# Kernel tuning notes

Measured on AMD Instinct MI355X. Metric: run time of the kernel, lower is better.

## Reference

```python
import jax, jax.numpy as jnp
import numpy as np

B, D, C, L, H = 4096, 768, 512, 32, 256
E = C * L  # total flattened extension embeddings

def _l2norm(x, eps=1e-12):
    n = jnp.sqrt(jnp.sum(x * x, axis=-1, keepdims=True))
    return x / jnp.maximum(n, eps)

def setup_inputs() -> dict:
    key = jax.random.key(0)
    ks = jax.random.split(key, 8)
    text_feat = jax.random.normal(ks[0], (B, D), dtype=jnp.float32)
    img_feat = jax.random.normal(ks[1], (B, D), dtype=jnp.float32)
    ext_embs = _l2norm(jax.random.normal(ks[2], (E, D), dtype=jnp.float32))
    concept_names = _l2norm(jax.random.normal(ks[3], (C, D), dtype=jnp.float32))
    # each concept has exactly L extension embeddings; sorted segment ids
    segment_ids = jnp.repeat(jnp.arange(C, dtype=jnp.int32), L)
    W1 = jax.random.normal(ks[4], (C + D, H), dtype=jnp.float32) * (1.0 / np.sqrt(C + D))
    b1 = jnp.zeros((H,), dtype=jnp.float32)
    W2 = jax.random.normal(ks[5], (H, C), dtype=jnp.float32) * (1.0 / np.sqrt(H))
    b2 = jnp.zeros((C,), dtype=jnp.float32)
    alpha = jnp.float32(0.5)
    temperature = jnp.float32(0.07)
    return {"text_feat": text_feat, "img_feat": img_feat, "ext_embs": ext_embs,
            "segment_ids": segment_ids, "concept_names": concept_names,
            "W1": W1, "b1": b1, "W2": W2, "b2": b2,
            "alpha": alpha, "temperature": temperature}

def reference(text_feat, img_feat, ext_embs, segment_ids, concept_names,
              W1, b1, W2, b2, alpha, temperature):
    # query = normalize(text + img)
    q = _l2norm(text_feat + img_feat)                      # [B, D]
    # ragged per-concept max similarity: one big GEMM + segmented max
    sim = jnp.einsum('bd,ed->be', q, ext_embs)            # [B, E]
    prior = jax.ops.segment_max(sim.T, segment_ids,
                                num_segments=C,
                                indices_are_sorted=True).T  # [B, C]
    # small MLP -> temperature softmax -> weighted concept sum
    h = jax.nn.relu(jnp.concatenate([prior, q], axis=-1) @ W1 + b1)  # [B, H]
    logits = h @ W2 + b2                                   # [B, C]
    weights = jax.nn.softmax(logits / temperature, axis=-1)
    dyn_prompt = weights @ concept_names                   # [B, D]
    combined = text_feat + alpha * dyn_prompt
    return _l2norm(combined)
```

## Files before the change

kernel.cpp:

```cpp
#include <hip/hip_runtime.h>
#include <hip/hip_bf16.h>

typedef unsigned short bfu;
typedef __attribute__((ext_vector_type(4))) float f32x4;
typedef __attribute__((ext_vector_type(8))) short bf16x8;
typedef __attribute__((ext_vector_type(4))) int i32x4;
typedef __attribute__((ext_vector_type(8))) int i32x8;

__device__ __forceinline__ unsigned short f2bf(float f) {
    unsigned int u = __float_as_uint(f);
    u += 0x7FFFu + ((u >> 16) & 1u);
    return (unsigned short)(u >> 16);
}

__device__ __forceinline__ unsigned pack_fp8x4(float a, float b, float c, float d) {
    int u = __builtin_amdgcn_cvt_pk_fp8_f32(a, b, 0, false);
    u = __builtin_amdgcn_cvt_pk_fp8_f32(c, d, u, true);
    return (unsigned)u;
}

__device__ __forceinline__ void gload_lds16(const void* g, void* l) {
    __builtin_amdgcn_global_load_lds(
        (const __attribute__((address_space(1))) unsigned int*)g,
        (__attribute__((address_space(3))) unsigned int*)l, 16, 0, 0);
}

__device__ __forceinline__ float block_sum256(float v, float* sm) {
    #pragma unroll
    for (int off = 32; off; off >>= 1) v += __shfl_xor(v, off);
    int w = threadIdx.x >> 6;
    if ((threadIdx.x & 63) == 0) sm[w] = v;
    __syncthreads();
    float r = sm[0] + sm[1] + sm[2] + sm[3];
    __syncthreads();
    return r;
}

__device__ __forceinline__ float block_max256(float v, float* sm) {
    #pragma unroll
    for (int off = 32; off; off >>= 1) v = fmaxf(v, __shfl_xor(v, off));
    int w = threadIdx.x >> 6;
    if ((threadIdx.x & 63) == 0) sm[w] = v;
    __syncthreads();
    float r = fmaxf(fmaxf(sm[0], sm[1]), fmaxf(sm[2], sm[3]));
    __syncthreads();
    return r;
}

__global__ __launch_bounds__(256) void prep_kernel(const float* __restrict__ text,
                                                   const float* __restrict__ img,
                                                   bfu* __restrict__ X,
                                                   unsigned* __restrict__ Q8,
                                                   const float* __restrict__ ext,
                                                   unsigned* __restrict__ E8,
                                                   const float* __restrict__ W1, bfu* __restrict__ W1t,
                                                   const float* __restrict__ W2, bfu* __restrict__ W2t,
                                                   const float* __restrict__ cn, bfu* __restrict__ cnt) {
    __shared__ float sm[4];
    int b = blockIdx.x, t = threadIdx.x;
    if (b < 4096) {
        int row = b;
        float4 v = {0.f, 0.f, 0.f, 0.f};
        if (t < 192) {
            float4 a = ((const float4*)(text + (size_t)row * 768))[t];
            float4 c = ((const float4*)(img + (size_t)row * 768))[t];
            v.x = a.x + c.x; v.y = a.y + c.y; v.z = a.z + c.z; v.w = a.w + c.w;
        }
        float ss = v.x * v.x + v.y * v.y + v.z * v.z + v.w * v.w;
        float tot = block_sum256(ss, sm);
        float inv = 1.0f / fmaxf(sqrtf(tot), 1e-12f);
        if (t < 192) {
            ushort4 o = make_ushort4(f2bf(v.x * inv), f2bf(v.y * inv), f2bf(v.z * inv), f2bf(v.w * inv));
            ((ushort4*)(X + (size_t)row * 1280 + 512))[t] = o;
            float s16 = inv * 16.0f;
            Q8[(size_t)row * 192 + t] = pack_fp8x4(v.x * s16, v.y * s16, v.z * s16, v.w * s16);
        }
    } else if (b < 16384) {
        int i = (b - 4096) * 256 + t;
        float4 v = ((const float4*)ext)[i];
        E8[i] = pack_fp8x4(v.x * 16.0f, v.y * 16.0f, v.z * 16.0f, v.w * 16.0f);
    } else if (b < 17664) {
        int idx = (b - 16384) * 256 + t;
        int c = idx / 1280, r = idx - c * 1280;
        W1t[idx] = f2bf(W1[(size_t)r * 256 + c]);
    } else if (b < 18176) {
        int idx = (b - 17664) * 256 + t;
        int c = idx / 256, r = idx - c * 256;
        W2t[idx] = f2bf(W2[(size_t)r * 512 + c]);
    } else {
        int idx = (b - 18176) * 256 + t;
        int c = idx / 512, r = idx - c * 512;
        cnt[idx] = f2bf(cn[(size_t)r * 768 + c]);
    }
}

__device__ __forceinline__ i32x8 ld_frag8(const char* s, int row, int lq) {
    const int r7 = row & 7;
    i32x4 lo = *(const i32x4*)(s + row * 128 + ((((lq << 1))     ^ r7) << 4));
    i32x4 hi = *(const i32x4*)(s + row * 128 + ((((lq << 1) | 1) ^ r7) << 4));
    i32x8 v;
    v[0] = lo[0]; v[1] = lo[1]; v[2] = lo[2]; v[3] = lo[3];
    v[4] = hi[0]; v[5] = hi[1]; v[6] = hi[2]; v[7] = hi[3];
    return v;
}

__global__ __launch_bounds__(256, 1) void sim_segmax_kernel(const unsigned char* __restrict__ Q8,
                                                            const unsigned char* __restrict__ E8,
                                                            bfu* __restrict__ X) {
    __shared__ __align__(16) char sA[2][128 * 128];
    __shared__ __align__(16) char sB[2][128 * 128];
    const int bm = blockIdx.x & 31;
    const int bn = blockIdx.x >> 5;
    const int m0 = bm << 7, n0 = bn << 7;
    const int t = threadIdx.x, lane = t & 63, wv = t >> 6;
    const int wm = (wv >> 1) << 6;
    const int wn = (wv & 1) << 6;
    const int lr = lane & 15, lq = lane >> 4;

    f32x4 zero = {0.f, 0.f, 0.f, 0.f};
    f32x4 acc[4][4];
    #pragma unroll
    for (int i = 0; i < 4; ++i)
        #pragma unroll
        for (int j = 0; j < 4; ++j) acc[i][j] = zero;

    auto stageA = [&](char* buf, int k0, int i) {
        int idx = (i << 8) + t;
        int row = idx >> 3, c = idx & 7;
        int cs = c ^ (row & 7);
        gload_lds16(Q8 + (size_t)(m0 + row) * 768 + k0 + (cs << 4),
                    buf + (((i << 8) + (wv << 6)) << 4));
    };
    auto stageB = [&](char* buf, int k0, int i) {
        int idx = (i << 8) + t;
        int row = idx >> 3, c = idx & 7;
        int cs = c ^ (row & 7);
        gload_lds16(E8 + (size_t)(n0 + row) * 768 + k0 + (cs << 4),
                    buf + (((i << 8) + (wv << 6)) << 4));
    };

    #pragma unroll
    for (int i = 0; i < 4; ++i) stageA(sA[0], 0, i);
    #pragma unroll
    for (int i = 0; i < 4; ++i) stageB(sB[0], 0, i);
    __syncthreads();

    for (int kk = 0; kk < 6; ++kk) {
        if (kk) __syncthreads();
        const char* bufA = sA[kk & 1];
        const char* bufB = sB[kk & 1];
        if (kk < 5) {
            char* nxA = sA[(kk & 1) ^ 1];
            char* nxB = sB[(kk & 1) ^ 1];
            const int k0n = (kk + 1) << 7;
            #pragma unroll
            for (int i = 0; i < 4; ++i) stageA(nxA, k0n, i);
            #pragma unroll
            for (int i = 0; i < 4; ++i) stageB(nxB, k0n, i);
        }
        i32x8 af[4], bf[4];
        #pragma unroll
        for (int f = 0; f < 4; ++f)
            af[f] = ld_frag8(bufA, wm + f * 16 + lr, lq);
        #pragma unroll
        for (int f = 0; f < 4; ++f)
            bf[f] = ld_frag8(bufB, wn + f * 16 + lr, lq);
        #pragma unroll
        for (int i = 0; i < 4; ++i)
            #pragma unroll
            for (int j = 0; j < 4; ++j)
                acc[i][j] = __builtin_amdgcn_mfma_scale_f32_16x16x128_f8f6f4(
                    af[i], bf[j], acc[i][j], 0, 0, 0, 0x7F7F7F7F, 0, 0x7F7F7F7F);
    }

    const float sc = 0.00390625f;
    const int gbase = (n0 + wn) >> 5;
    #pragma unroll
    for (int g = 0; g < 2; ++g) {
        #pragma unroll
        for (int i = 0; i < 4; ++i) {
            #pragma unroll
            for (int r = 0; r < 4; ++r) {
                float v = fmaxf(acc[i][2 * g][r], acc[i][2 * g + 1][r]);
                #pragma unroll
                for (int off = 8; off; off >>= 1)
                    v = fmaxf(v, __shfl_xor(v, off));
                if (lr == 0) {
                    int row = m0 + wm + i * 16 + lq * 4 + r;
                    X[(size_t)row * 1280 + gbase + g] = f2bf(v * sc);
                }
            }
        }
    }
}

template <int BM>
__device__ __forceinline__ void gemm_mainloop(const bfu* A, const bfu* B, int K,
                                              int lda, int ldb, int m0, int n0,
                                              short* sA, short* sB, f32x4 acc[BM / 32][4]) {
    const int t = threadIdx.x, lane = t & 63, wv = t >> 6;
    const int wm = (wv >> 1) * (BM / 2), wn = (wv & 1) << 6;
    const int lr = lane & 15, lq = lane >> 4;

    i32x4 ra[BM / 32], rb[4];
    auto ldg = [&](int k0) {
        #pragma unroll
        for (int i = 0; i < BM / 32; ++i) {
            int idx = i * 256 + t;
            int row = idx >> 3, cg = idx & 7;
            ra[i] = *(const i32x4*)(A + (size_t)(m0 + row) * lda + k0 + (cg << 3));
        }
        #pragma unroll
        for (int i = 0; i < 4; ++i) {
            int idx = i * 256 + t;
            int row = idx >> 3, cg = idx & 7;
            rb[i] = *(const i32x4*)(B + (size_t)(n0 + row) * ldb + k0 + (cg << 3));
        }
    };
    auto st_lds = [&]() {
        #pragma unroll
        for (int i = 0; i < BM / 32; ++i) {
            int idx = i * 256 + t;
            int row = idx >> 3, cg = idx & 7, cs = cg ^ (row & 7);
            *(i32x4*)(sA + row * 64 + cs * 8) = ra[i];
        }
        #pragma unroll
        for (int i = 0; i < 4; ++i) {
            int idx = i * 256 + t;
            int row = idx >> 3, cg = idx & 7, cs = cg ^ (row & 7);
            *(i32x4*)(sB + row * 64 + cs * 8) = rb[i];
        }
    };

    const int NIT = K >> 6;
    ldg(0);
    for (int kk = 0; kk < NIT; ++kk) {
        if (kk) __syncthreads();
        st_lds();
        __syncthreads();
        if (kk + 1 < NIT) ldg((kk + 1) * 64);
        #pragma unroll
        for (int ks = 0; ks < 2; ++ks) {
            bf16x8 af[BM / 32], bfr[4];
            #pragma unroll
            for (int f = 0; f < BM / 32; ++f) {
                int mrow = wm + f * 16 + lr;
                int c = ks * 4 + lq;
                af[f] = *(const bf16x8*)(sA + mrow * 64 + ((c ^ (mrow & 7)) << 3));
            }
            #pragma unroll
            for (int f = 0; f < 4; ++f) {
                int nrow = wn + f * 16 + lr;
                int c = ks * 4 + lq;
                bfr[f] = *(const bf16x8*)(sB + nrow * 64 + ((c ^ (nrow & 7)) << 3));
            }
            #pragma unroll
            for (int i = 0; i < BM / 32; ++i)
                #pragma unroll
                for (int j = 0; j < 4; ++j)
                    acc[i][j] = __builtin_amdgcn_mfma_f32_16x16x32_bf16(af[i], bfr[j], acc[i][j], 0, 0, 0);
        }
    }
}

template <int EPI, int BM>
__global__ __launch_bounds__(256) void gemm_kernel(const bfu* __restrict__ A,
                                                   const bfu* __restrict__ B,
                                                   const float* __restrict__ bias,
                                                   void* __restrict__ out,
                                                   int K, int lda, int ldb, int N, int ntN) {
    __shared__ __align__(16) short sA[BM * 64];
    __shared__ __align__(16) short sB[128 * 64];
    int bm = blockIdx.x / ntN, bn = blockIdx.x - bm * ntN;
    int m0 = bm * BM, n0 = bn * 128;
    f32x4 zero = {0.f, 0.f, 0.f, 0.f};
    f32x4 acc[BM / 32][4];
    #pragma unroll
    for (int i = 0; i < BM / 32; ++i)
        #pragma unroll
        for (int j = 0; j < 4; ++j) acc[i][j] = zero;

    gemm_mainloop<BM>(A, B, K, lda, ldb, m0, n0, sA, sB, acc);

    const int t = threadIdx.x, lane = t & 63, wv = t >> 6;
    const int wm = (wv >> 1) * (BM / 2), wn = (wv & 1) << 6;
    const int lr = lane & 15, lq = lane >> 4;
    #pragma unroll
    for (int j = 0; j < 4; ++j) {
        int col = n0 + wn + j * 16 + lr;
        float bv = (EPI >= 1) ? bias[col] : 0.0f;
        #pragma unroll
        for (int i = 0; i < BM / 32; ++i) {
            #pragma unroll
            for (int r = 0; r < 4; ++r) {
                int row = m0 + wm + i * 16 + lq * 4 + r;
                float v = acc[i][j][r] + bv;
                if (EPI == 1) {
                    v = fmaxf(v, 0.0f);
                    ((bfu*)out)[(size_t)row * N + col] = f2bf(v);
                } else {
                    ((float*)out)[(size_t)row * N + col] = v;
                }
            }
        }
    }
}

__global__ __launch_bounds__(256) void softmax_kernel(const float* __restrict__ logits,
                                                      const float* __restrict__ temp,
                                                      bfu* __restrict__ wout) {
    __shared__ float sm[4];
    int row = blockIdx.x, t = threadIdx.x;
    float invT = 1.0f / temp[0];
    float l0 = logits[(size_t)row * 512 + t];
    float l1 = logits[(size_t)row * 512 + 256 + t];
    float m = block_max256(fmaxf(l0, l1), sm);
    float e0 = __expf((l0 - m) * invT);
    float e1 = __expf((l1 - m) * invT);
    float s = block_sum256(e0 + e1, sm);
    float inv = 1.0f / s;
    wout[(size_t)row * 512 + t]       = f2bf(e0 * inv);
    wout[(size_t)row * 512 + 256 + t] = f2bf(e1 * inv);
}

__global__ __launch_bounds__(256) void final_kernel(const float* __restrict__ text,
                                                    const float* __restrict__ dyn,
                                                    const float* __restrict__ alpha,
                                                    float* __restrict__ out) {
    __shared__ float sm[4];
    int row = blockIdx.x, t = threadIdx.x;
    float a = alpha[0];
    float v[3]; float ss = 0.f;
    #pragma unroll
    for (int i = 0; i < 3; ++i) {
        size_t o = (size_t)row * 768 + t + 256 * i;
        v[i] = text[o] + a * dyn[o];
        ss += v[i] * v[i];
    }
    float tot = block_sum256(ss, sm);
    float inv = 1.0f / fmaxf(sqrtf(tot), 1e-12f);
    #pragma unroll
    for (int i = 0; i < 3; ++i)
        out[(size_t)row * 768 + t + 256 * i] = v[i] * inv;
}

extern "C" void kernel_launch(void* const* d_in, const int* in_sizes, int n_in,
                              void* d_out, int out_size, void* d_ws, size_t ws_size,
                              hipStream_t stream) {
    const float* text  = (const float*)d_in[0];
    const float* img   = (const float*)d_in[1];
    const float* ext   = (const float*)d_in[2];
    const float* cn    = (const float*)d_in[4];
    const float* W1    = (const float*)d_in[5];
    const float* b1    = (const float*)d_in[6];
    const float* W2    = (const float*)d_in[7];
    const float* b2    = (const float*)d_in[8];
    const float* alpha = (const float*)d_in[9];
    const float* temp  = (const float*)d_in[10];
    float* out = (float*)d_out;

    char* p = (char*)d_ws;
    auto carve = [&](size_t bytes) -> char* {
        char* r = p; p += (bytes + 255) & ~(size_t)255; return r;
    };
    unsigned char* E8 = (unsigned char*)carve((size_t)16384 * 768);
    unsigned char* Q8 = (unsigned char*)carve((size_t)4096 * 768);
    bfu*   X      = (bfu*)carve((size_t)4096 * 1280 * 2);
    bfu*   W1t    = (bfu*)carve((size_t)256 * 1280 * 2);
    bfu*   W2t    = (bfu*)carve((size_t)512 * 256 * 2);
    bfu*   cnt    = (bfu*)carve((size_t)768 * 512 * 2);
    bfu*   Hm     = (bfu*)carve((size_t)4096 * 256 * 2);
    float* logits = (float*)carve((size_t)4096 * 512 * 4);
    bfu*   wts    = (bfu*)carve((size_t)4096 * 512 * 2);
    float* dyn    = (float*)carve((size_t)4096 * 768 * 4);

    prep_kernel<<<19712, 256, 0, stream>>>(text, img, X, (unsigned*)Q8,
                                           ext, (unsigned*)E8, W1, W1t, W2, W2t, cn, cnt);
    sim_segmax_kernel<<<4096, 256, 0, stream>>>(Q8, E8, X);
    gemm_kernel<1, 64><<<64 * 2, 256, 0, stream>>>(X, W1t, b1, (void*)Hm, 1280, 1280, 1280, 256, 2);
    gemm_kernel<2, 64><<<64 * 4, 256, 0, stream>>>(Hm, W2t, b2, (void*)logits, 256, 256, 256, 512, 4);
    softmax_kernel<<<4096, 256, 0, stream>>>(logits, temp, wts);
    gemm_kernel<0, 64><<<64 * 6, 256, 0, stream>>>(wts, cnt, nullptr, (void*)dyn, 512, 512, 512, 768, 6);
    final_kernel<<<4096, 256, 0, stream>>>(text, dyn, alpha, out);
}
```

Measured before the change: 329.1 us.

## Triple-buffer LDS staging in sim GEMM with explicit vmcnt waits

Moves the fp8 similarity GEMM from double to triple LDS buffering, so global-to-LDS loads run two K-steps ahead of the MFMAs. Each step waits only on its oldest load group with partial `s_waitcnt vmcnt` counts instead of a full `__syncthreads`. The K loop is fully unrolled, and `sched_barrier` fences stop the compiler from reordering around the waits. This aims to hide global load latency on a short six-step K loop. The cost is a larger LDS footprint and fragile hand-coded wait counts that are tied to the number of loads per stage.

```diff
diff --git a/kernel.cpp b/kernel.cpp
--- a/kernel.cpp
+++ b/kernel.cpp
@@ -107,8 +107,8 @@
 __global__ __launch_bounds__(256, 1) void sim_segmax_kernel(const unsigned char* __restrict__ Q8,
                                                             const unsigned char* __restrict__ E8,
                                                             bfu* __restrict__ X) {
-    __shared__ __align__(16) char sA[2][128 * 128];
-    __shared__ __align__(16) char sB[2][128 * 128];
+    __shared__ __align__(16) char sA[3][128 * 128];
+    __shared__ __align__(16) char sB[3][128 * 128];
     const int bm = blockIdx.x & 31;
     const int bn = blockIdx.x >> 5;
     const int m0 = bm << 7, n0 = bn << 7;
@@ -138,26 +138,26 @@
         gload_lds16(E8 + (size_t)(n0 + row) * 768 + k0 + (cs << 4),
                     buf + (((i << 8) + (wv << 6)) << 4));
     };
-
-    #pragma unroll
-    for (int i = 0; i < 4; ++i) stageA(sA[0], 0, i);
-    #pragma unroll
-    for (int i = 0; i < 4; ++i) stageB(sB[0], 0, i);
-    __syncthreads();
-
+    auto stage = [&](char* bufA, char* bufB, int k0) {
+        #pragma unroll
+        for (int i = 0; i < 4; ++i) stageA(bufA, k0, i);
+        #pragma unroll
+        for (int i = 0; i < 4; ++i) stageB(bufB, k0, i);
+    };
+
+    stage(sA[0], sB[0], 0);
+    stage(sA[1], sB[1], 128);
+    __builtin_amdgcn_sched_barrier(0);
+    asm volatile("s_waitcnt vmcnt(8)" ::: "memory");
+    __builtin_amdgcn_sched_barrier(0);
+    __builtin_amdgcn_s_barrier();
+    __builtin_amdgcn_sched_barrier(0);
+
+    #pragma unroll
     for (int kk = 0; kk < 6; ++kk) {
-        if (kk) __syncthreads();
-        const char* bufA = sA[kk & 1];
-        const char* bufB = sB[kk & 1];
-        if (kk < 5) {
-            char* nxA = sA[(kk & 1) ^ 1];
-            char* nxB = sB[(kk & 1) ^ 1];
-            const int k0n = (kk + 1) << 7;
-            #pragma unroll
-            for (int i = 0; i < 4; ++i) stageA(nxA, k0n, i);
-            #pragma unroll
-            for (int i = 0; i < 4; ++i) stageB(nxB, k0n, i);
-        }
+        if (kk < 4) stage(sA[(kk + 2) % 3], sB[(kk + 2) % 3], (kk + 2) << 7);
+        const char* bufA = sA[kk % 3];
+        const char* bufB = sB[kk % 3];
         i32x8 af[4], bf[4];
         #pragma unroll
         for (int f = 0; f < 4; ++f)
@@ -171,6 +171,15 @@
             for (int j = 0; j < 4; ++j)
                 acc[i][j] = __builtin_amdgcn_mfma_scale_f32_16x16x128_f8f6f4(
                     af[i], bf[j], acc[i][j], 0, 0, 0, 0x7F7F7F7F, 0, 0x7F7F7F7F);
+        if (kk < 5) {
+            __builtin_amdgcn_sched_barrier(0);
+            if (kk < 4)  asm volatile("s_waitcnt vmcnt(8)" ::: "memory");
+            else         asm volatile("s_waitcnt vmcnt(0)" ::: "memory");
+            asm volatile("s_waitcnt lgkmcnt(0)" ::: "memory");
+            __builtin_amdgcn_sched_barrier(0);
+            __builtin_amdgcn_s_barrier();
+            __builtin_amdgcn_sched_barrier(0);
+        }
     }
 
     const float sc = 0.00390625f;
```

Result: faster. 318.4 us (-3.3%).
